# Kernel tuning notes

Measured on AMD Instinct MI355X. Metric: run time of the kernel, lower is better.

## Reference

```python
import jax, jax.numpy as jnp
import numpy as np

NUM_HEADS = 16
ROPE_THETA = 10000.0


def _rope_angles(seq_len, head_dim, dtype):
    # lucidrains rotary_embedding_torch: freqs = theta^(-2i/d) for i in 0..d/2,
    # angles = pos * freq, then each angle repeated twice along last dim (interleaved pairs).
    inv_freq = 1.0 / (ROPE_THETA ** (jnp.arange(0, head_dim, 2, dtype=jnp.float32) / head_dim))
    angles = jnp.arange(seq_len, dtype=jnp.float32)[:, None] * inv_freq  # [N, D/2]
    return jnp.repeat(angles, 2, axis=-1).astype(dtype)  # [N, D]


def _rotate_half(t):
    # interleaved pairs: (x0, x1) -> (-x1, x0)
    t1 = t[..., ::2]
    t2 = t[..., 1::2]
    return jnp.stack([-t2, t1], axis=-1).reshape(t.shape)


def _apply_rope(t, cos, sin):
    # t: [B, H, N, D]; cos/sin: [N, D]
    return t * cos + _rotate_half(t) * sin


def setup_inputs() -> dict:
    key = jax.random.key(0)
    ks = jax.random.split(key, 5)
    B, N, C = 4, 1024, 1024
    return {
        "x": jax.random.normal(ks[0], (B, N, C), dtype=jnp.float32),
        "w_qkv": jax.random.normal(ks[1], (C, 3 * C), dtype=jnp.float32) * (C ** -0.5),
        "b_qkv": jax.random.normal(ks[2], (3 * C,), dtype=jnp.float32) * 0.02,
        "w_proj": jax.random.normal(ks[3], (C, C), dtype=jnp.float32) * (C ** -0.5),
        "b_proj": jax.random.normal(ks[4], (C,), dtype=jnp.float32) * 0.02,
    }


def reference(x, w_qkv, b_qkv, w_proj, b_proj):
    B, N, C = x.shape
    H = NUM_HEADS
    D = C // H

    qkv = x @ w_qkv + b_qkv  # [B, N, 3C]
    qkv = qkv.reshape(B, N, 3, H, D).transpose(2, 0, 3, 1, 4)  # [3, B, H, N, D]
    q, k, v = qkv[0], qkv[1], qkv[2]

    ang = _rope_angles(N, D, x.dtype)
    cos, sin = jnp.cos(ang), jnp.sin(ang)
    q = _apply_rope(q, cos, sin)
    k = _apply_rope(k, cos, sin)

    scale = D ** -0.5  # SDPA default scale
    scores = jnp.einsum("bhqd,bhkd->bhqk", q, k) * scale
    attn = jax.nn.softmax(scores, axis=-1)
    out = jnp.einsum("bhqk,bhkd->bhqd", attn, v)  # [B, H, N, D]

    out = out.transpose(0, 2, 1, 3).reshape(B, N, C)
    return out @ w_proj + b_proj
```

## Files before the change

kernel.cpp:

```cpp
#include <hip/hip_runtime.h>
#include <math.h>

#define BB 4
#define NN 1024
#define CC 1024
#define HH 16
#define DD 64
#define N3 3072

typedef __attribute__((ext_vector_type(8))) short bf16x8;
typedef __attribute__((ext_vector_type(8))) _Float16 f16x8;
typedef __attribute__((ext_vector_type(4))) _Float16 f16x4;
typedef __attribute__((ext_vector_type(4))) float f32x4;
typedef __attribute__((ext_vector_type(4))) unsigned int u32x4;
typedef __attribute__((ext_vector_type(2))) unsigned int u32x2;

struct ushort4_t { unsigned short x, y, z, w; };

static __device__ __forceinline__ unsigned short f2b(float f) {
    union { float f; unsigned int u; } v; v.f = f;
    unsigned int r = (v.u + 0x7fffu + ((v.u >> 16) & 1u)) >> 16;
    return (unsigned short)r;
}

static __device__ __forceinline__ void ldg_lds16(const void* g, void* l) {
    __builtin_amdgcn_global_load_lds(
        (const __attribute__((address_space(1))) unsigned int*)g,
        (__attribute__((address_space(3))) unsigned int*)l, 16, 0, 0);
}

static __device__ __forceinline__ void barx()  { asm volatile("s_barrier" ::: "memory"); }
static __device__ __forceinline__ void wlg0()  { asm volatile("s_waitcnt lgkmcnt(0)" ::: "memory");
                                                 __builtin_amdgcn_sched_barrier(0); }
static __device__ __forceinline__ void wvm8()  { asm volatile("s_waitcnt vmcnt(8)" ::: "memory"); }
static __device__ __forceinline__ void wvm4()  { asm volatile("s_waitcnt vmcnt(4)" ::: "memory"); }
static __device__ __forceinline__ void wvm2()  { asm volatile("s_waitcnt vmcnt(2)" ::: "memory"); }
static __device__ __forceinline__ void wvm0()  { asm volatile("s_waitcnt vmcnt(0)" ::: "memory"); }
static __device__ __forceinline__ void wnone() {}

__global__ __launch_bounds__(256) void prep(const float* __restrict__ x,
                                            const float* __restrict__ wq,
                                            const float* __restrict__ wp,
                                            _Float16* __restrict__ Xh,
                                            _Float16* __restrict__ Wqt,
                                            _Float16* __restrict__ Wpt,
                                            float* __restrict__ ct,
                                            float* __restrict__ st) {
    __shared__ __align__(16) _Float16 T[64][72];
    const int blk = blockIdx.x;
    const int t = threadIdx.x;
    if (blk < 4096) {
        int tid = blk * 256 + t;
        float4 v = ((const float4*)x)[tid];
        f16x4 o = {(_Float16)v.x, (_Float16)v.y, (_Float16)v.z, (_Float16)v.w};
        ((f16x4*)Xh)[tid] = o;
    } else if (blk < 5120) {
        const float* src; _Float16* dst; int ns, k0, n0;
        if (blk < 4864) {
            int idx = blk - 4096;
            k0 = (idx & 15) * 64; n0 = (idx >> 4) * 64;
            src = wq; dst = Wqt; ns = N3;
        } else {
            int idx = blk - 4864;
            k0 = (idx & 15) * 64; n0 = (idx >> 4) * 64;
            src = wp; dst = Wpt; ns = 1024;
        }
        {
            const int r  = t >> 2;
            const int cf = (t & 3) * 16;
            const float* sp = src + (size_t)(k0 + r) * ns + n0 + cf;
            float4 v0 = *(const float4*)(sp);
            float4 v1 = *(const float4*)(sp + 4);
            float4 v2 = *(const float4*)(sp + 8);
            float4 v3 = *(const float4*)(sp + 12);
            f16x8 a, b;
            a[0]=(_Float16)v0.x; a[1]=(_Float16)v0.y; a[2]=(_Float16)v0.z; a[3]=(_Float16)v0.w;
            a[4]=(_Float16)v1.x; a[5]=(_Float16)v1.y; a[6]=(_Float16)v1.z; a[7]=(_Float16)v1.w;
            b[0]=(_Float16)v2.x; b[1]=(_Float16)v2.y; b[2]=(_Float16)v2.z; b[3]=(_Float16)v2.w;
            b[4]=(_Float16)v3.x; b[5]=(_Float16)v3.y; b[6]=(_Float16)v3.z; b[7]=(_Float16)v3.w;
            *(f16x8*)&T[r][cf]     = a;
            *(f16x8*)&T[r][cf + 8] = b;
        }
        __syncthreads();
        {
            const int n  = t >> 2;
            const int kc = t & 3;
            f16x8 o0, o1;
            #pragma unroll
            for (int kk = 0; kk < 8; kk++) o0[kk] = T[kc * 16 + kk][n];
            #pragma unroll
            for (int kk = 0; kk < 8; kk++) o1[kk] = T[kc * 16 + 8 + kk][n];
            _Float16* dp = dst + (size_t)(n0 + n) * 1024 + k0 + kc * 16;
            *(f16x8*)dp       = o0;
            *(f16x8*)(dp + 8) = o1;
        }
    } else {
        int tid = (blk - 5120) * 256 + t;
        int n = tid >> 5, i = tid & 31;
        double ang = (double)n * exp2(-(double)i * (13.287712379549449 / 32.0));
        ct[tid] = (float)cos(ang);
        st[tid] = (float)sin(ang);
    }
}

__global__ __launch_bounds__(512, 2) void qkv_mfma(const _Float16* __restrict__ Ah,
                                                   const _Float16* __restrict__ Bt,
                                                   const float* __restrict__ bias,
                                                   const float* __restrict__ cost,
                                                   const float* __restrict__ sint,
                                                   unsigned short* __restrict__ Q,
                                                   unsigned short* __restrict__ K,
                                                   unsigned short* __restrict__ Vtg) {
    __shared__ __align__(16) _Float16 LA[4][128 * 64];
    __shared__ __align__(16) _Float16 LB[4][128 * 64];

    const int t    = threadIdx.x;
    const int lane = t & 63;
    const int w    = t >> 6;
    const int ln   = lane & 15, qd = lane >> 4;
    const int n0   = blockIdx.x * 256;
    const int m0   = blockIdx.y * 256;
    const int wm   = (w >> 2) * 128;
    const int wn   = (w & 3) * 64;

    const int L0 = t >> 3, hc0 = (t & 7) ^ (L0 & 7);
    const int row0 = 2 * L0 + (hc0 >> 2), co0 = (hc0 & 3) * 16;
    const int pp = 512 + t;
    const int L1 = pp >> 3, hc1 = (pp & 7) ^ (L1 & 7);
    const int row1 = 2 * L1 + (hc1 >> 2), co1 = (hc1 & 3) * 16;

    const char* gA = (const char*)Ah;
    const char* gB = (const char*)Bt;
    const size_t aof0 = (size_t)(m0 + row0) * 2048 + co0;
    const size_t aof1 = (size_t)(m0 + row1) * 2048 + co1;
    const size_t bof0 = (size_t)(n0 + row0) * 2048 + co0;
    const size_t bof1 = (size_t)(n0 + row1) * 2048 + co1;
    const int ld0 = (w * 64) * 8;
    const int ld1 = (512 + w * 64) * 8;

#define STAGE_A(kk, SLOT) { ldg_lds16(gA + aof0 + (size_t)(kk) * 64, &LA[SLOT][ld0]); \
                            ldg_lds16(gA + aof1 + (size_t)(kk) * 64, &LA[SLOT][ld1]); }
#define STAGE_B(kk, SLOT) { ldg_lds16(gB + bof0 + (size_t)(kk) * 64, &LB[SLOT][ld0]); \
                            ldg_lds16(gB + bof1 + (size_t)(kk) * 64, &LB[SLOT][ld1]); }

    STAGE_A(0, 0); STAGE_B(0, 0);
    STAGE_A(1, 1); STAGE_B(1, 1);
    STAGE_A(2, 2); STAGE_B(2, 2);
    wvm8();
    barx();

    f32x4 acc[8][4];
    #pragma unroll
    for (int i = 0; i < 8; i++)
        #pragma unroll
        for (int j = 0; j < 4; j++) acc[i][j] = (f32x4){0.f, 0.f, 0.f, 0.f};

    auto frag = [&](const _Float16* Lb, int r, int c) -> f16x8 {
        int idx = ((r >> 1) << 6) + ((((((r & 1) << 2) | c)) ^ ((r >> 1) & 7)) << 3);
        return *(const f16x8*)&Lb[idx];
    };

#define QK_TILE(kk, SLOT, STG, WAITFN) {                                            \
    const _Float16* Ab = LA[SLOT];                                                  \
    const _Float16* Bb = LB[SLOT];                                                  \
    f16x8 af[4], bf[4];                                                             \
    _Pragma("unroll") for (int i = 0; i < 4; i++) af[i] = frag(Ab, wm + i * 16 + ln, qd); \
    _Pragma("unroll") for (int j = 0; j < 4; j++) bf[j] = frag(Bb, wn + j * 16 + ln, qd); \
    if (STG) STAGE_A((kk) + 3, ((kk) + 3) & 3);                                     \
    barx(); wlg0();                                                                 \
    __builtin_amdgcn_s_setprio(1);                                                  \
    _Pragma("unroll") for (int i = 0; i < 4; i++)                                   \
        _Pragma("unroll") for (int j = 0; j < 4; j++)                               \
            acc[i][j] = __builtin_amdgcn_mfma_f32_16x16x32_f16(af[i], bf[j], acc[i][j], 0, 0, 0); \
    __builtin_amdgcn_s_setprio(0);                                                  \
    barx();                                                                         \
    _Pragma("unroll") for (int i = 0; i < 4; i++) af[i] = frag(Ab, wm + 64 + i * 16 + ln, qd); \
    if (STG) STAGE_B((kk) + 3, ((kk) + 3) & 3);                                     \
    WAITFN();                                                                       \
    barx(); wlg0();                                                                 \
    __builtin_amdgcn_s_setprio(1);                                                  \
    _Pragma("unroll") for (int i = 0; i < 4; i++)                                   \
        _Pragma("unroll") for (int j = 0; j < 4; j++)                               \
            acc[4 + i][j] = __builtin_amdgcn_mfma_f32_16x16x32_f16(af[i], bf[j], acc[4 + i][j], 0, 0, 0); \
    __builtin_amdgcn_s_setprio(0);                                                  \
    barx();                                                                         \
}

    for (int k = 0; k < 28; k += 4) {
        QK_TILE(k + 0, 0, 1, wvm8);
        QK_TILE(k + 1, 1, 1, wvm8);
        QK_TILE(k + 2, 2, 1, wvm8);
        QK_TILE(k + 3, 3, 1, wvm8);
    }
    QK_TILE(28, 0, 1, wvm8);
    QK_TILE(29, 1, 0, wvm4);
    QK_TILE(30, 2, 0, wvm0);
    QK_TILE(31, 3, 0, wnone);

#undef QK_TILE
#undef STAGE_A
#undef STAGE_B

    float* LW = (float*)(&LA[0][0]) + w * (16 * 68);
    const int s = (n0 + wn) >> 10;
    const int h = ((n0 + wn) >> 6) & 15;
    const int erow = lane >> 2;
    const int ec0  = (lane & 3) * 16;

    if (s < 2) {
        unsigned short* dst = (s == 0) ? Q : K;
        const float sc0 = (s == 0) ? 0.125f : 1.0f;
        f32x4 bb0 = *(const f32x4*)&bias[n0 + wn + ec0 + 0];
        f32x4 bb1 = *(const f32x4*)&bias[n0 + wn + ec0 + 4];
        f32x4 bb2 = *(const f32x4*)&bias[n0 + wn + ec0 + 8];
        f32x4 bb3 = *(const f32x4*)&bias[n0 + wn + ec0 + 12];
        #pragma unroll
        for (int i = 0; i < 8; i++) {
            #pragma unroll
            for (int j = 0; j < 4; j++)
                #pragma unroll
                for (int reg = 0; reg < 4; reg++)
                    LW[(qd * 4 + reg) * 68 + j * 16 + ln] = acc[i][j][reg];
            wlg0();
            f32x4 v0 = *(const f32x4*)&LW[erow * 68 + ec0 + 0];
            f32x4 v1 = *(const f32x4*)&LW[erow * 68 + ec0 + 4];
            f32x4 v2 = *(const f32x4*)&LW[erow * 68 + ec0 + 8];
            f32x4 v3 = *(const f32x4*)&LW[erow * 68 + ec0 + 12];
            wlg0();
            int row = m0 + wm + i * 16 + erow;
            int b = row >> 10, n = row & 1023;
            f32x4 cs0 = *(const f32x4*)&cost[n * 32 + (ec0 >> 1)];
            f32x4 cs1 = *(const f32x4*)&cost[n * 32 + (ec0 >> 1) + 4];
            f32x4 sn0 = *(const f32x4*)&sint[n * 32 + (ec0 >> 1)];
            f32x4 sn1 = *(const f32x4*)&sint[n * 32 + (ec0 >> 1) + 4];
            cs0 *= sc0; cs1 *= sc0; sn0 *= sc0; sn1 *= sc0;
            v0 += bb0; v1 += bb1; v2 += bb2; v3 += bb3;
            unsigned int pk0, pk1, pk2, pk3, pk4, pk5, pk6, pk7;
#define RP(PK, ve, vo, cs, sn) { float oe = (ve) * (cs) - (vo) * (sn);              \
                                 float oo = (vo) * (cs) + (ve) * (sn);              \
            asm("v_cvt_pk_bf16_f32 %0, %1, %2" : "=v"(PK) : "v"(oe), "v"(oo)); }
            RP(pk0, v0[0], v0[1], cs0[0], sn0[0]);
            RP(pk1, v0[2], v0[3], cs0[1], sn0[1]);
            RP(pk2, v1[0], v1[1], cs0[2], sn0[2]);
            RP(pk3, v1[2], v1[3], cs0[3], sn0[3]);
            RP(pk4, v2[0], v2[1], cs1[0], sn1[0]);
            RP(pk5, v2[2], v2[3], cs1[1], sn1[1]);
            RP(pk6, v3[0], v3[1], cs1[2], sn1[2]);
            RP(pk7, v3[2], v3[3], cs1[3], sn1[3]);
#undef RP
            unsigned short* op = dst + (((size_t)(b * HH + h)) * NN + n) * DD + ec0;
            u32x4 o0; o0[0] = pk0; o0[1] = pk1; o0[2] = pk2; o0[3] = pk3;
            u32x4 o1; o1[0] = pk4; o1[1] = pk5; o1[2] = pk6; o1[3] = pk7;
            *(u32x4*)op = o0;
            *(u32x4*)(op + 8) = o1;
        }
    } else {
        const float bb = bias[n0 + wn + lane];
        #pragma unroll
        for (int i = 0; i < 8; i++) {
            #pragma unroll
            for (int j = 0; j < 4; j++)
                #pragma unroll
                for (int reg = 0; reg < 4; reg++)
                    LW[(qd * 4 + reg) * 68 + j * 16 + ln] = acc[i][j][reg];
            wlg0();
            float e0  = LW[ 0 * 68 + lane] + bb, e1  = LW[ 1 * 68 + lane] + bb;
            float e2  = LW[ 2 * 68 + lane] + bb, e3  = LW[ 3 * 68 + lane] + bb;
            float e4  = LW[ 4 * 68 + lane] + bb, e5  = LW[ 5 * 68 + lane] + bb;
            float e6  = LW[ 6 * 68 + lane] + bb, e7  = LW[ 7 * 68 + lane] + bb;
            float e8  = LW[ 8 * 68 + lane] + bb, e9  = LW[ 9 * 68 + lane] + bb;
            float e10 = LW[10 * 68 + lane] + bb, e11 = LW[11 * 68 + lane] + bb;
            float e12 = LW[12 * 68 + lane] + bb, e13 = LW[13 * 68 + lane] + bb;
            float e14 = LW[14 * 68 + lane] + bb, e15 = LW[15 * 68 + lane] + bb;
            wlg0();
            unsigned int pk0, pk1, pk2, pk3, pk4, pk5, pk6, pk7;
#define CV(PK, a, b_) asm("v_cvt_pk_bf16_f32 %0, %1, %2" : "=v"(PK) : "v"(a), "v"(b_))
            CV(pk0, e0,  e1);  CV(pk1, e2,  e3);
            CV(pk2, e4,  e5);  CV(pk3, e6,  e7);
            CV(pk4, e8,  e9);  CV(pk5, e10, e11);
            CV(pk6, e12, e13); CV(pk7, e14, e15);
#undef CV
            int row0v = m0 + wm + i * 16;
            int b = row0v >> 10, nn = row0v & 1023;
            unsigned short* vp = Vtg + ((size_t)(b * HH + h) * DD + lane) * NN + nn;
            u32x4 o0; o0[0] = pk0; o0[1] = pk1; o0[2] = pk2; o0[3] = pk3;
            u32x4 o1; o1[0] = pk4; o1[1] = pk5; o1[2] = pk6; o1[3] = pk7;
            *(u32x4*)vp = o0;
            *(u32x4*)(vp + 8) = o1;
        }
    }
}

__global__ __launch_bounds__(256, 3) void attn_flash(const unsigned short* __restrict__ Qb,
                                                     const unsigned short* __restrict__ Kb,
                                                     const unsigned short* __restrict__ Vtg,
                                                     _Float16* __restrict__ AO) {
    __shared__ __align__(16) unsigned short Ks[2][64 * 64];
    __shared__ __align__(16) unsigned short Vt[2][64 * 64];
    __shared__ __align__(16) unsigned short Ps[4][32 * 64];

    const int t    = threadIdx.x;
    const int lane = t & 63;
    const int w    = t >> 6;
    const int ln   = lane & 15;
    const int qd   = lane >> 4;

    const int lin  = blockIdx.x;
    const int slot = lin >> 3;
    const int hb   = (lin & 7) + 8 * (slot & 7);
    const int bq   = slot >> 3;
    const int h    = hb & 15;
    const int b    = hb >> 4;

    const size_t base = (size_t)(b * HH + h) * NN * DD;
    const char* Kc = (const char*)(Kb + base);
    const char* Vc = (const char*)(Vtg + base);
    const int xorc = ((lane & 7) ^ (lane >> 3)) * 16;
    const int r8   = lane >> 3;
    const int wrow = w * 16;

    bf16x8 qf[2][2];
    #pragma unroll
    for (int g = 0; g < 2; g++) {
        const unsigned short* qp = Qb + base +
            (size_t)(bq * 128 + w * 32 + g * 16 + ln) * DD + qd * 8;
        qf[g][0] = *(const bf16x8*)qp;
        qf[g][1] = *(const bf16x8*)(qp + 32);
    }

    f32x4 o[2][5];
    #pragma unroll
    for (int g = 0; g < 2; g++)
        #pragma unroll
        for (int x = 0; x < 5; x++) o[g][x] = (f32x4){0.f, 0.f, 0.f, 0.f};

    bf16x8 onesf;
    #pragma unroll
    for (int x = 0; x < 8; x++) onesf[x] = (short)0x3F80;

#define STAGE_K(tile, buf) {                                                     \
    _Pragma("unroll") for (int c = 0; c < 2; c++) {                              \
        int rr = wrow + c * 8 + r8;                                              \
        ldg_lds16(Kc + (size_t)((tile) * 64 + rr) * 128 + xorc,                  \
                  &Ks[buf][(wrow + c * 8) * 64]);                                \
    } }
#define STAGE_V(tile, buf) {                                                     \
    _Pragma("unroll") for (int c = 0; c < 2; c++) {                              \
        int rr = wrow + c * 8 + r8;                                              \
        ldg_lds16(Vc + (size_t)rr * 2048 + (size_t)(tile) * 128 + xorc,          \
                  &Vt[buf][(wrow + c * 8) * 64]);                                \
    } }

    STAGE_K(0, 0); STAGE_V(0, 0);
    STAGE_K(1, 1); STAGE_V(1, 1);

    const float C1 = 1.44269504f;
    const float C0 = -16.0f * 1.44269504f;
    const int swp = 2 * (ln & 7);
    unsigned short* PsB = &Ps[w][0];

    #pragma unroll
    for (int tt = 0; tt < 16; tt++) {
        if (tt < 15) wvm4(); else wvm0();
        barx();

        const unsigned short* KsB = Ks[tt & 1];
        const unsigned short* VtB = Vt[tt & 1];

        f32x4 s[2][4];
        #pragma unroll
        for (int j = 0; j < 4; j++) {
            bf16x8 k0f = *(const bf16x8*)&KsB[(ln + 16 * j) * 64 + ((qd ^ (ln & 7)) * 8)];
            bf16x8 k1f = *(const bf16x8*)&KsB[(ln + 16 * j) * 64 + (((4 + qd) ^ (ln & 7)) * 8)];
            #pragma unroll
            for (int g = 0; g < 2; g++) {
                f32x4 sj = {0.f, 0.f, 0.f, 0.f};
                sj = __builtin_amdgcn_mfma_f32_16x16x32_bf16(k0f, qf[g][0], sj, 0, 0, 0);
                sj = __builtin_amdgcn_mfma_f32_16x16x32_bf16(k1f, qf[g][1], sj, 0, 0, 0);
                s[g][j] = sj;
            }
        }

        #pragma unroll
        for (int g = 0; g < 2; g++) {
            char* rowp = (char*)PsB + (g * 16 + ln) * 128;
            #pragma unroll
            for (int j = 0; j < 4; j++) {
                float p0, p1, p2, p3;
                float x0 = fmaf(s[g][j][0], C1, C0);
                float x1 = fmaf(s[g][j][1], C1, C0);
                float x2 = fmaf(s[g][j][2], C1, C0);
                float x3 = fmaf(s[g][j][3], C1, C0);
                asm("v_exp_f32 %0, %1" : "=v"(p0) : "v"(x0));
                asm("v_exp_f32 %0, %1" : "=v"(p1) : "v"(x1));
                asm("v_exp_f32 %0, %1" : "=v"(p2) : "v"(x2));
                asm("v_exp_f32 %0, %1" : "=v"(p3) : "v"(x3));
                unsigned int lo, hi;
                asm("v_cvt_pk_bf16_f32 %0, %1, %2" : "=v"(lo) : "v"(p0), "v"(p1));
                asm("v_cvt_pk_bf16_f32 %0, %1, %2" : "=v"(hi) : "v"(p2), "v"(p3));
                u32x2 pk; pk[0] = lo; pk[1] = hi;
                *(u32x2*)(rowp + (((4 * j + qd) ^ swp) * 8)) = pk;
            }
        }

        {
            bf16x8 pf[2][2];
            #pragma unroll
            for (int g = 0; g < 2; g++) {
                pf[g][0] = *(const bf16x8*)&PsB[(g * 16 + ln) * 64 + ((qd ^ (ln & 7)) * 8)];
                pf[g][1] = *(const bf16x8*)&PsB[(g * 16 + ln) * 64 + (((4 + qd) ^ (ln & 7)) * 8)];
            }
            __builtin_amdgcn_s_setprio(1);
            #pragma unroll
            for (int j = 0; j < 4; j++) {
                bf16x8 v0f = *(const bf16x8*)&VtB[(ln + 16 * j) * 64 + ((qd ^ (ln & 7)) * 8)];
                bf16x8 v1f = *(const bf16x8*)&VtB[(ln + 16 * j) * 64 + (((4 + qd) ^ (ln & 7)) * 8)];
                #pragma unroll
                for (int g = 0; g < 2; g++) {
                    o[g][j] = __builtin_amdgcn_mfma_f32_16x16x32_bf16(pf[g][0], v0f, o[g][j], 0, 0, 0);
                    o[g][j] = __builtin_amdgcn_mfma_f32_16x16x32_bf16(pf[g][1], v1f, o[g][j], 0, 0, 0);
                }
            }
            #pragma unroll
            for (int g = 0; g < 2; g++) {
                o[g][4] = __builtin_amdgcn_mfma_f32_16x16x32_bf16(pf[g][0], onesf, o[g][4], 0, 0, 0);
                o[g][4] = __builtin_amdgcn_mfma_f32_16x16x32_bf16(pf[g][1], onesf, o[g][4], 0, 0, 0);
            }
            __builtin_amdgcn_s_setprio(0);
        }

        barx();

        if (tt < 14) {
            STAGE_K(tt + 2, tt & 1);
            STAGE_V(tt + 2, tt & 1);
        }
    }

#undef STAGE_K
#undef STAGE_V

    #pragma unroll
    for (int g = 0; g < 2; g++)
        #pragma unroll
        for (int r = 0; r < 4; r++) {
            float inv = __builtin_amdgcn_rcpf(o[g][4][r]);
            int q = bq * 128 + w * 32 + g * 16 + qd * 4 + r;
            _Float16* op = AO + (((size_t)b * NN + q) * HH + h) * DD + ln;
            op[0]  = (_Float16)(o[g][0][r] * inv);
            op[16] = (_Float16)(o[g][1][r] * inv);
            op[32] = (_Float16)(o[g][2][r] * inv);
            op[48] = (_Float16)(o[g][3][r] * inv);
        }
}

__global__ __launch_bounds__(512, 2) void proj_mfma(const _Float16* __restrict__ Ah,
                                                    const _Float16* __restrict__ Bt,
                                                    const float* __restrict__ bias,
                                                    float* __restrict__ out) {
    __shared__ __align__(16) _Float16 LA[4][128 * 32];
    __shared__ __align__(16) _Float16 LB[4][128 * 32];

    const int t    = threadIdx.x;
    const int lane = t & 63;
    const int w    = t >> 6;
    const int ln   = lane & 15, qd = lane >> 4;
    const int n0   = blockIdx.x * 128;
    const int m0   = blockIdx.y * 128;
    const int wm   = (w >> 2) * 64;
    const int wn   = (w & 3) * 32;

    const int L  = t >> 3, hc = (t & 7) ^ (L & 7);
    const int row = 2 * L + (hc >> 2), co = (hc & 3) * 16;
    const char* gA = (const char*)Ah;
    const char* gB = (const char*)Bt;
    const size_t aof = (size_t)(m0 + row) * 2048 + co;
    const size_t bof = (size_t)(n0 + row) * 2048 + co;
    const int ld = (w * 64) * 8;

#define PSTAGE(kk, SLOT) { ldg_lds16(gA + aof + (size_t)(kk) * 64, &LA[SLOT][ld]); \
                           ldg_lds16(gB + bof + (size_t)(kk) * 64, &LB[SLOT][ld]); }

    PSTAGE(0, 0); PSTAGE(1, 1); PSTAGE(2, 2);
    wvm4();
    barx();

    f32x4 acc[4][2];
    #pragma unroll
    for (int i = 0; i < 4; i++)
        #pragma unroll
        for (int j = 0; j < 2; j++) acc[i][j] = (f32x4){0.f, 0.f, 0.f, 0.f};

    auto frag = [&](const _Float16* Lb, int r, int c) -> f16x8 {
        int idx = ((r >> 1) << 6) + ((((((r & 1) << 2) | c)) ^ ((r >> 1) & 7)) << 3);
        return *(const f16x8*)&Lb[idx];
    };

#define PTILE(kk, SLOT, STG, WAITFN) {                                              \
    const _Float16* Ab = LA[SLOT];                                                  \
    const _Float16* Bb = LB[SLOT];                                                  \
    f16x8 af[4], bf[2];                                                             \
    _Pragma("unroll") for (int i = 0; i < 4; i++) af[i] = frag(Ab, wm + i * 16 + ln, qd); \
    _Pragma("unroll") for (int j = 0; j < 2; j++) bf[j] = frag(Bb, wn + j * 16 + ln, qd); \
    if (STG) PSTAGE((kk) + 3, ((kk) + 3) & 3);                                      \
    WAITFN();                                                                       \
    barx(); wlg0();                                                                 \
    __builtin_amdgcn_s_setprio(1);                                                  \
    _Pragma("unroll") for (int i = 0; i < 4; i++)                                   \
        _Pragma("unroll") for (int j = 0; j < 2; j++)                               \
            acc[i][j] = __builtin_amdgcn_mfma_f32_16x16x32_f16(af[i], bf[j], acc[i][j], 0, 0, 0); \
    __builtin_amdgcn_s_setprio(0);                                                  \
    barx();                                                                         \
}

    for (int k = 0; k < 28; k += 4) {
        PTILE(k + 0, 0, 1, wvm4);
        PTILE(k + 1, 1, 1, wvm4);
        PTILE(k + 2, 2, 1, wvm4);
        PTILE(k + 3, 3, 1, wvm4);
    }
    PTILE(28, 0, 1, wvm4);
    PTILE(29, 1, 0, wvm2);
    PTILE(30, 2, 0, wvm0);
    PTILE(31, 3, 0, wnone);

#undef PTILE
#undef PSTAGE

    const float bc0 = bias[n0 + wn + ln];
    const float bc1 = bias[n0 + wn + 16 + ln];
    #pragma unroll
    for (int i = 0; i < 4; i++) {
        #pragma unroll
        for (int reg = 0; reg < 4; reg++) {
            int rowo = m0 + wm + i * 16 + qd * 4 + reg;
            float* op = out + (size_t)rowo * 1024 + n0 + wn + ln;
            op[0]  = acc[i][0][reg] + bc0;
            op[16] = acc[i][1][reg] + bc1;
        }
    }
}

extern "C" void kernel_launch(void* const* d_in, const int* in_sizes, int n_in,
                              void* d_out, int out_size, void* d_ws, size_t ws_size,
                              hipStream_t stream) {
    const float* x      = (const float*)d_in[0];
    const float* w_qkv  = (const float*)d_in[1];
    const float* b_qkv  = (const float*)d_in[2];
    const float* w_proj = (const float*)d_in[3];
    const float* b_proj = (const float*)d_in[4];
    float* out = (float*)d_out;

    char* ws = (char*)d_ws;
    _Float16* Xh   = (_Float16*)(ws);
    _Float16* Wqt  = (_Float16*)(ws + (8u << 20));
    _Float16* Wpt  = (_Float16*)(ws + (14u << 20));
    unsigned short* Q  = (unsigned short*)(ws + (16u << 20));
    unsigned short* K  = (unsigned short*)(ws + (24u << 20));
    unsigned short* Vt = (unsigned short*)(ws + (32u << 20));
    _Float16* AOh  = (_Float16*)(ws + (40u << 20));
    float* cost    = (float*)(ws + (48u << 20));
    float* sint    = (float*)(ws + (48u << 20) + (128u << 10));

    prep<<<5248, 256, 0, stream>>>(x, w_qkv, w_proj, Xh, Wqt, Wpt, cost, sint);
    qkv_mfma<<<dim3(12, 16), 512, 0, stream>>>(Xh, Wqt, b_qkv, cost, sint, Q, K, Vt);
    attn_flash<<<512, 256, 0, stream>>>(Q, K, Vt, AOh);
    proj_mfma<<<dim3(8, 32), 512, 0, stream>>>(AOh, Wpt, b_proj, out);
}
```

Measured before the change: 161.4 us.

## Software-pipeline QK^T one tile ahead with triple-buffered K in flash attention

The attention loop now computes the QK^T scores for tile tt+1 while the exp and PV work for tile tt runs, so matrix-core work can overlap the transcendental and LDS traffic. K moves to a three-deep LDS ring so the next tile's K is already resident. The custom vmcnt waits and barriers are replaced by one __syncthreads per iteration. LDS per block grows and launch bounds drop from 3 to 2 blocks per CU. That lowers occupancy and raises register pressure from holding two score sets, and the full sync may serialize loads that were overlapped before.

```diff
diff --git a/kernel.cpp b/kernel.cpp
--- a/kernel.cpp
+++ b/kernel.cpp
@@ -291,11 +291,11 @@
     }
 }
 
-__global__ __launch_bounds__(256, 3) void attn_flash(const unsigned short* __restrict__ Qb,
+__global__ __launch_bounds__(256, 2) void attn_flash(const unsigned short* __restrict__ Qb,
                                                      const unsigned short* __restrict__ Kb,
                                                      const unsigned short* __restrict__ Vtg,
                                                      _Float16* __restrict__ AO) {
-    __shared__ __align__(16) unsigned short Ks[2][64 * 64];
+    __shared__ __align__(16) unsigned short Ks[3][64 * 64];
     __shared__ __align__(16) unsigned short Vt[2][64 * 64];
     __shared__ __align__(16) unsigned short Ps[4][32 * 64];
 
@@ -338,21 +338,40 @@
     #pragma unroll
     for (int x = 0; x < 8; x++) onesf[x] = (short)0x3F80;
 
-#define STAGE_K(tile, buf) {                                                     \
-    _Pragma("unroll") for (int c = 0; c < 2; c++) {                              \
-        int rr = wrow + c * 8 + r8;                                              \
-        ldg_lds16(Kc + (size_t)((tile) * 64 + rr) * 128 + xorc,                  \
-                  &Ks[buf][(wrow + c * 8) * 64]);                                \
-    } }
-#define STAGE_V(tile, buf) {                                                     \
-    _Pragma("unroll") for (int c = 0; c < 2; c++) {                              \
-        int rr = wrow + c * 8 + r8;                                              \
-        ldg_lds16(Vc + (size_t)rr * 2048 + (size_t)(tile) * 128 + xorc,          \
-                  &Vt[buf][(wrow + c * 8) * 64]);                                \
-    } }
-
-    STAGE_K(0, 0); STAGE_V(0, 0);
-    STAGE_K(1, 1); STAGE_V(1, 1);
+    #pragma unroll
+    for (int tile = 0; tile < 3; tile++)
+        #pragma unroll
+        for (int c = 0; c < 2; c++) {
+            int rr = wrow + c * 8 + r8;
+            ldg_lds16(Kc + (size_t)(tile * 64 + rr) * 128 + xorc,
+                      &Ks[tile][(wrow + c * 8) * 64]);
+        }
+    #pragma unroll
+    for (int tile = 0; tile < 2; tile++)
+        #pragma unroll
+        for (int c = 0; c < 2; c++) {
+            int rr = wrow + c * 8 + r8;
+            ldg_lds16(Vc + (size_t)rr * 2048 + (size_t)tile * 128 + xorc,
+                      &Vt[tile][(wrow + c * 8) * 64]);
+        }
+    __syncthreads();
+
+    f32x4 scur[2][4];
+    {
+        const unsigned short* KsB = Ks[0];
+        #pragma unroll
+        for (int j = 0; j < 4; j++) {
+            bf16x8 k0f = *(const bf16x8*)&KsB[(ln + 16 * j) * 64 + ((qd ^ (ln & 7)) * 8)];
+            bf16x8 k1f = *(const bf16x8*)&KsB[(ln + 16 * j) * 64 + (((4 + qd) ^ (ln & 7)) * 8)];
+            #pragma unroll
+            for (int g = 0; g < 2; g++) {
+                f32x4 sj = {0.f, 0.f, 0.f, 0.f};
+                sj = __builtin_amdgcn_mfma_f32_16x16x32_bf16(k0f, qf[g][0], sj, 0, 0, 0);
+                sj = __builtin_amdgcn_mfma_f32_16x16x32_bf16(k1f, qf[g][1], sj, 0, 0, 0);
+                scur[g][j] = sj;
+            }
+        }
+    }
 
     const float C1 = 1.44269504f;
     const float C0 = -16.0f * 1.44269504f;
@@ -361,24 +380,23 @@
 
     #pragma unroll
     for (int tt = 0; tt < 16; tt++) {
-        if (tt < 15) wvm4(); else wvm0();
-        barx();
-
-        const unsigned short* KsB = Ks[tt & 1];
-        const unsigned short* VtB = Vt[tt & 1];
-
-        f32x4 s[2][4];
-        #pragma unroll
-        for (int j = 0; j < 4; j++) {
-            bf16x8 k0f = *(const bf16x8*)&KsB[(ln + 16 * j) * 64 + ((qd ^ (ln & 7)) * 8)];
-            bf16x8 k1f = *(const bf16x8*)&KsB[(ln + 16 * j) * 64 + (((4 + qd) ^ (ln & 7)) * 8)];
-            #pragma unroll
-            for (int g = 0; g < 2; g++) {
-                f32x4 sj = {0.f, 0.f, 0.f, 0.f};
-                sj = __builtin_amdgcn_mfma_f32_16x16x32_bf16(k0f, qf[g][0], sj, 0, 0, 0);
-                sj = __builtin_amdgcn_mfma_f32_16x16x32_bf16(k1f, qf[g][1], sj, 0, 0, 0);
-                s[g][j] = sj;
-            }
+        f32x4 snext[2][4];
+        if (tt < 15) {
+            const unsigned short* KsB = Ks[(tt + 1) % 3];
+            __builtin_amdgcn_s_setprio(1);
+            #pragma unroll
+            for (int j = 0; j < 4; j++) {
+                bf16x8 k0f = *(const bf16x8*)&KsB[(ln + 16 * j) * 64 + ((qd ^ (ln & 7)) * 8)];
+                bf16x8 k1f = *(const bf16x8*)&KsB[(ln + 16 * j) * 64 + (((4 + qd) ^ (ln & 7)) * 8)];
+                #pragma unroll
+                for (int g = 0; g < 2; g++) {
+                    f32x4 sj = {0.f, 0.f, 0.f, 0.f};
+                    sj = __builtin_amdgcn_mfma_f32_16x16x32_bf16(k0f, qf[g][0], sj, 0, 0, 0);
+                    sj = __builtin_amdgcn_mfma_f32_16x16x32_bf16(k1f, qf[g][1], sj, 0, 0, 0);
+                    snext[g][j] = sj;
+                }
+            }
+            __builtin_amdgcn_s_setprio(0);
         }
 
         #pragma unroll
@@ -387,10 +405,10 @@
             #pragma unroll
             for (int j = 0; j < 4; j++) {
                 float p0, p1, p2, p3;
-                float x0 = fmaf(s[g][j][0], C1, C0);
-                float x1 = fmaf(s[g][j][1], C1, C0);
-                float x2 = fmaf(s[g][j][2], C1, C0);
-                float x3 = fmaf(s[g][j][3], C1, C0);
+                float x0 = fmaf(scur[g][j][0], C1, C0);
+                float x1 = fmaf(scur[g][j][1], C1, C0);
+                float x2 = fmaf(scur[g][j][2], C1, C0);
+                float x3 = fmaf(scur[g][j][3], C1, C0);
                 asm("v_exp_f32 %0, %1" : "=v"(p0) : "v"(x0));
                 asm("v_exp_f32 %0, %1" : "=v"(p1) : "v"(x1));
                 asm("v_exp_f32 %0, %1" : "=v"(p2) : "v"(x2));
@@ -404,6 +422,7 @@
         }
 
         {
+            const unsigned short* VtB = Vt[tt & 1];
             bf16x8 pf[2][2];
             #pragma unroll
             for (int g = 0; g < 2; g++) {
@@ -429,16 +448,32 @@
             __builtin_amdgcn_s_setprio(0);
         }
 
-        barx();
-
-        if (tt < 14) {
-            STAGE_K(tt + 2, tt & 1);
-            STAGE_V(tt + 2, tt & 1);
-        }
-    }
-
-#undef STAGE_K
-#undef STAGE_V
+        __syncthreads();
+
+        if (tt <= 12) {
+            int tile = tt + 3;
+            #pragma unroll
+            for (int c = 0; c < 2; c++) {
+                int rr = wrow + c * 8 + r8;
+                ldg_lds16(Kc + (size_t)(tile * 64 + rr) * 128 + xorc,
+                          &Ks[tt % 3][(wrow + c * 8) * 64]);
+            }
+        }
+        if (tt <= 13) {
+            int tile = tt + 2;
+            #pragma unroll
+            for (int c = 0; c < 2; c++) {
+                int rr = wrow + c * 8 + r8;
+                ldg_lds16(Vc + (size_t)rr * 2048 + (size_t)tile * 128 + xorc,
+                          &Vt[tt & 1][(wrow + c * 8) * 64]);
+            }
+        }
+
+        #pragma unroll
+        for (int g = 0; g < 2; g++)
+            #pragma unroll
+            for (int j = 0; j < 4; j++) scur[g][j] = snext[g][j];
+    }
 
     #pragma unroll
     for (int g = 0; g < 2; g++)
```

After: 162.1 us. About the same (+0.5%).
